# Kernel tuning notes

Hardware: AMD Instinct MI355X
Metric: run time of the kernel (lower is better)

Reference implementation:

```python
import jax, jax.numpy as jnp
import numpy as np

B, A, C, M = 4, 120000, 80, 32
ALPHA, GAMMA, EPS = 0.75, 2.0, 1e-4
STD = np.array([0.1, 0.1, 0.2, 0.2, 0.1, 0.1, 0.2, 0.2], dtype=np.float32)


def _make_boxes(key, shape, img=1024.0):
    k1, k2, k3, k4 = jax.random.split(key, 4)
    cx = jax.random.uniform(k1, shape) * img
    cy = jax.random.uniform(k2, shape) * img
    w = jax.random.uniform(k3, shape) * 224.0 + 32.0
    h = jax.random.uniform(k4, shape) * 224.0 + 32.0
    return jnp.stack([cx - 0.5 * w, cy - 0.5 * h, cx + 0.5 * w, cy + 0.5 * h], axis=-1)


def setup_inputs() -> dict:
    key = jax.random.key(0)
    kc, kr, ka, kh, kf, kl, ki = jax.random.split(key, 7)
    classifications = jax.random.uniform(kc, (B, A, C), dtype=jnp.float32)
    regressions = jax.random.normal(kr, (B, A, 8), dtype=jnp.float32)
    anchors = _make_boxes(ka, (1, A))  # [1,A,4]
    head = _make_boxes(kh, (B, M))     # [B,M,4]
    full = _make_boxes(kf, (B, M))     # [B,M,4]
    labels = jax.random.randint(kl, (B, M, 1), 0, C).astype(jnp.float32)
    ignore = jax.random.randint(ki, (B, M, 1), 0, 2).astype(jnp.float32)
    annotations = jnp.concatenate([head, full, labels, ignore], axis=-1)  # [B,M,10]
    return {"classifications": classifications, "regressions": regressions,
            "anchors": anchors, "annotations": annotations}


def _calc_iou(a, b):
    # a: [A,4], b: [B,M,4] -> [B,A,M]
    area_b = (b[..., 2] - b[..., 0]) * (b[..., 3] - b[..., 1])  # [B,M]
    a = a[None, :, None, :]
    bb = b[:, None, :, :]
    iw = jnp.clip(jnp.minimum(a[..., 2], bb[..., 2]) - jnp.maximum(a[..., 0], bb[..., 0]), 0.0)
    ih = jnp.clip(jnp.minimum(a[..., 3], bb[..., 3]) - jnp.maximum(a[..., 1], bb[..., 1]), 0.0)
    area_a = ((a[..., 2] - a[..., 0]) * (a[..., 3] - a[..., 1]))  # [1,A,1]
    inter = iw * ih
    ua = jnp.clip(area_a + area_b[:, None, :] - inter, 1e-8)
    return inter / ua


def reference(classifications, regressions, anchors, annotations):
    anchor = anchors[0]                       # [A,4]
    aw = anchor[:, 2] - anchor[:, 0]
    ah = anchor[:, 3] - anchor[:, 1]
    acx = anchor[:, 0] + 0.5 * aw
    acy = anchor[:, 1] + 0.5 * ah

    ann = annotations[..., :-1]               # [B,M,9]
    full_box = ann[..., 4:8]

    iou = _calc_iou(anchor, full_box)         # [B,A,M]
    iou_max = jnp.max(iou, axis=-1)           # [B,A]
    iou_arg = jnp.argmax(iou, axis=-1)        # [B,A]

    pos = iou_max >= 0.5                      # [B,A]
    neg = iou_max < 0.4
    num_pos = jnp.sum(pos, axis=1).astype(jnp.float32)  # [B]

    assigned = jnp.take_along_axis(ann, iou_arg[..., None], axis=1)  # [B,A,9]
    assigned_cls = assigned[..., 8].astype(jnp.int32)                # [B,A]

    one_hot = jax.nn.one_hot(assigned_cls, classifications.shape[-1], dtype=jnp.float32)
    targets = jnp.where(pos[..., None], one_hot,
                        jnp.where(neg[..., None], 0.0, -1.0))        # [B,A,C]

    p = jnp.clip(classifications, EPS, 1.0 - EPS)
    alpha_f = jnp.where(targets == 1.0, ALPHA, 1.0 - ALPHA)
    focal_w = alpha_f * jnp.where(targets == 1.0, 1.0 - p, p) ** GAMMA
    bce = -(targets * jnp.log(p) + (1.0 - targets) * jnp.log(1.0 - p))
    cls_loss = jnp.where(targets != -1.0, focal_w * bce, 0.0)
    cls_losses = jnp.sum(cls_loss, axis=(1, 2)) / jnp.clip(num_pos, 1.0)  # [B]

    gw_h = assigned[..., 2] - assigned[..., 0]
    gh_h = assigned[..., 3] - assigned[..., 1]
    gcx_h = assigned[..., 0] + 0.5 * gw_h
    gcy_h = assigned[..., 1] + 0.5 * gh_h
    gw_f = assigned[..., 6] - assigned[..., 4]
    gh_f = assigned[..., 7] - assigned[..., 5]
    gcx_f = assigned[..., 4] + 0.5 * gw_f
    gcy_f = assigned[..., 5] + 0.5 * gh_f
    gw_h = jnp.clip(gw_h, 1.0); gh_h = jnp.clip(gh_h, 1.0)
    gw_f = jnp.clip(gw_f, 1.0); gh_f = jnp.clip(gh_f, 1.0)

    t = jnp.stack([
        (gcx_f - acx) / aw, (gcy_f - acy) / ah,
        jnp.log(gw_f / aw), jnp.log(gh_f / ah),
        (gcx_h - acx) / aw * 4.0, (gcy_h - acy) / ah * 4.0,
        jnp.log(gw_h / aw * 4.0), jnp.log(gh_h / ah * 4.0),
    ], axis=-1) / jnp.asarray(STD)            # [B,A,8]

    diff = jnp.abs(t - regressions)
    # only_full=True: weights zero out cols 4:8
    diff = diff * jnp.asarray([1., 1., 1., 1., 0., 0., 0., 0.], dtype=jnp.float32)
    rl = jnp.where(diff <= 1.0 / 9.0, 0.5 * 9.0 * diff * diff, diff - 0.5 / 9.0)
    rl4 = rl[..., 0:4] * pos[..., None]       # [B,A,4], only positive anchors
    reg_losses = jnp.where(num_pos > 0,
                           jnp.sum(rl4, axis=(1, 2)) / (jnp.clip(num_pos, 1.0) * 4.0),
                           0.0)               # mean over positive rows x 4 cols

    return (jnp.mean(cls_losses, keepdims=True), jnp.mean(reg_losses, keepdims=True))
```

## Files before the change

kernel.cpp:

```cpp
#include <hip/hip_runtime.h>

#define NB 4
#define NA 120000
#define NC 80
#define NM 32

#define EPS_   1e-4f
#define LN2_   0.69314718055994531f

constexpr int BLOCK  = 256;
constexpr int WPB    = 4;
constexpr int APW    = 16;
constexpr int APC    = WPB * APW;
constexpr int NCHUNK = NA / APC;
constexpr int BPB    = 512;
constexpr int BINS   = 64;
constexpr int QCAP   = 256;

__device__ __forceinline__ float wave_reduce_f(float v) {
    #pragma unroll
    for (int off = 32; off > 0; off >>= 1) v += __shfl_down(v, off, 64);
    return v;
}
__device__ __forceinline__ double wave_reduce_d(double v) {
    #pragma unroll
    for (int off = 32; off > 0; off >>= 1) v += __shfl_down(v, off, 64);
    return v;
}

__device__ __forceinline__ float flog2(float x) { return __builtin_amdgcn_logf(x); }

__global__ __launch_bounds__(BLOCK, 4)
void focal_persist(const float* __restrict__ cls,
                   const float* __restrict__ reg,
                   const float* __restrict__ anchors,
                   const float* __restrict__ ann,
                   double* __restrict__ acc)
{
    __shared__ float s_ann[NM * 10];
    __shared__ float s_red[2][WPB];
    __shared__ int   s_q[QCAP];
    __shared__ int   s_qn;

    const int b    = blockIdx.x >> 9;
    const int blk  = blockIdx.x & (BPB - 1);
    const int tid  = threadIdx.x;
    const int wave = tid >> 6;
    const int lane = tid & 63;
    const int aloc = lane >> 2;
    const int part = lane & 3;

    if (tid == 0) s_qn = 0;
    s_ann[tid] = ann[b * NM * 10 + tid];
    if (tid < NM * 10 - BLOCK) s_ann[BLOCK + tid] = ann[b * NM * 10 + BLOCK + tid];
    __syncthreads();

    float clsSum = 0.0f, regLoss = 0.0f;

    const float4* anchors4 = (const float4*)anchors;
    const float4* cls4b    = (const float4*)cls + (size_t)b * NA * (NC / 4);

    int c = blk;
    float4 an0, x0, x1, x2, x3, x4_;
    {
        const int aw0 = c * APC + wave * APW;
        an0 = anchors4[aw0 + aloc];
        const float4* w4 = cls4b + (size_t)aw0 * (NC / 4);
        x0 = w4[lane]; x1 = w4[lane + 64]; x2 = w4[lane + 128];
        x3 = w4[lane + 192]; x4_ = w4[lane + 256];
    }

    while (c < NCHUNK) {
        const int cn = c + BPB;
        const int cl  = (cn < NCHUNK) ? cn : c;
        const int nw0 = cl * APC + wave * APW;
        const float4 an1 = anchors4[nw0 + aloc];
        const float4* v4 = cls4b + (size_t)nw0 * (NC / 4);
        const float4 y0 = v4[lane], y1 = v4[lane + 64], y2 = v4[lane + 128];
        const float4 y3 = v4[lane + 192], y4 = v4[lane + 256];

        const int a = c * APC + wave * APW + aloc;
        const float ax1 = an0.x, ay1 = an0.y, ax2 = an0.z, ay2 = an0.w;
        const float areaA = (ax2 - ax1) * (ay2 - ay1);

        float best = -1.0f;
        int   arg  = 0;
        #pragma unroll
        for (int i = 0; i < 8; ++i) {
            const int m = part * 8 + i;
            const float bx1 = s_ann[m * 10 + 4];
            const float by1 = s_ann[m * 10 + 5];
            const float bx2 = s_ann[m * 10 + 6];
            const float by2 = s_ann[m * 10 + 7];
            float iw = fminf(ax2, bx2) - fmaxf(ax1, bx1); iw = fmaxf(iw, 0.0f);
            float ih = fminf(ay2, by2) - fmaxf(ay1, by1); ih = fmaxf(ih, 0.0f);
            const float inter = iw * ih;
            const float areaB = (bx2 - bx1) * (by2 - by1);
            const float ua    = fmaxf(areaA + areaB - inter, 1e-8f);
            const float iou   = inter / ua;
            if (iou > best) { best = iou; arg = m; }
        }
        #pragma unroll
        for (int d = 1; d <= 2; d <<= 1) {
            const float ob = __shfl_xor(best, d, 64);
            const int   oa = __shfl_xor(arg,  d, 64);
            if (ob > best || (ob == best && oa < arg)) { best = ob; arg = oa; }
        }

        const bool pos = best >= 0.5f;
        const bool neg = best < 0.4f;
        const float coefL = (pos || neg) ? (-0.25f * LN2_) : 0.0f;

        if (pos && part == 0) {
            const int slot = atomicAdd(&s_qn, 1);
            s_q[slot] = (a << 5) | arg;
        }

        #define TERM(XV, J)                                                      \
        {                                                                        \
            const int idx = lane + 64 * (J);                                     \
            const float C = __shfl(coefL, (idx / (NC / 4)) << 2, 64);            \
            float p0 = fminf(fmaxf((XV).x, EPS_), 1.0f - EPS_);                  \
            float p1 = fminf(fmaxf((XV).y, EPS_), 1.0f - EPS_);                  \
            float p2 = fminf(fmaxf((XV).z, EPS_), 1.0f - EPS_);                  \
            float p3 = fminf(fmaxf((XV).w, EPS_), 1.0f - EPS_);                  \
            float t0 = p0 * p0 * flog2(1.0f - p0);                               \
            float t1 = p1 * p1 * flog2(1.0f - p1);                               \
            float t2 = p2 * p2 * flog2(1.0f - p2);                               \
            float t3 = p3 * p3 * flog2(1.0f - p3);                               \
            clsSum = fmaf((t0 + t1) + (t2 + t3), C, clsSum);                     \
        }
        TERM(x0, 0) TERM(x1, 1) TERM(x2, 2) TERM(x3, 3) TERM(x4_, 4)
        #undef TERM

        c = cn;
        an0 = an1; x0 = y0; x1 = y1; x2 = y2; x3 = y3; x4_ = y4;
    }

    __syncthreads();
    const int qn = s_qn;
    if (tid < qn) {
        const int e = s_q[tid];
        const int a = e >> 5;
        const int m = e & 31;

        const float4 an = anchors4[a];
        const float aw_ = an.z - an.x, ah = an.w - an.y;
        const float acx = an.x + 0.5f * aw_, acy = an.y + 0.5f * ah;

        const int cc = (int)s_ann[m * 10 + 8];
        const float xc = cls[((size_t)b * NA + a) * NC + cc];
        const float p  = fminf(fmaxf(xc, EPS_), 1.0f - EPS_);
        const float q  = 1.0f - p;
        clsSum += 0.75f * q * q * (-LN2_ * flog2(p))
                - 0.25f * p * p * (-LN2_ * flog2(q));

        const float fx1 = s_ann[m * 10 + 4];
        const float fy1 = s_ann[m * 10 + 5];
        const float fx2 = s_ann[m * 10 + 6];
        const float fy2 = s_ann[m * 10 + 7];
        float gw = fx2 - fx1, gh = fy2 - fy1;
        const float gcx = fx1 + 0.5f * gw, gcy = fy1 + 0.5f * gh;
        gw = fmaxf(gw, 1.0f); gh = fmaxf(gh, 1.0f);
        const float t0 = ((gcx - acx) / aw_) * 10.0f;
        const float t1 = ((gcy - acy) / ah)  * 10.0f;
        const float t2 = (LN2_ * flog2(gw / aw_)) * 5.0f;
        const float t3 = (LN2_ * flog2(gh / ah))  * 5.0f;
        const float4 r4 = ((const float4*)reg)[(size_t)(b * NA + a) * 2];
        const float d0 = fabsf(t0 - r4.x);
        const float d1 = fabsf(t1 - r4.y);
        const float d2 = fabsf(t2 - r4.z);
        const float d3 = fabsf(t3 - r4.w);
        const float beta = 1.0f / 9.0f;
        #define SL1(d) ((d) <= beta ? 4.5f * (d) * (d) : (d) - 0.5f / 9.0f)
        regLoss = SL1(d0) + SL1(d1) + SL1(d2) + SL1(d3);
        #undef SL1
    }

    float rc = wave_reduce_f(clsSum);
    float rr = wave_reduce_f(regLoss);
    if (lane == 0) { s_red[0][wave] = rc; s_red[1][wave] = rr; }
    __syncthreads();
    if (tid == 0) {
        const float cs = (s_red[0][0] + s_red[0][1]) + (s_red[0][2] + s_red[0][3]);
        const float rs = (s_red[1][0] + s_red[1][1]) + (s_red[1][2] + s_red[1][3]);
        const int bin = blockIdx.x & (BINS - 1);
        atomicAdd(&acc[(b * 3 + 0) * BINS + bin], (double)cs);
        atomicAdd(&acc[(b * 3 + 1) * BINS + bin], (double)rs);
        atomicAdd(&acc[(b * 3 + 2) * BINS + bin], (double)qn);
    }
}

__global__ void focal_finalize(const double* __restrict__ acc, float* __restrict__ out) {
    __shared__ double g[NB * 3];
    const int tid  = threadIdx.x;
    const int wave = tid >> 6, lane = tid & 63;
    double v = acc[wave * BINS + lane];
    v = wave_reduce_d(v);
    if (lane == 0) g[wave] = v;
    __syncthreads();
    if (tid == 0) {
        double clsTot = 0.0, regTot = 0.0;
        #pragma unroll
        for (int b = 0; b < NB; ++b) {
            const double np  = g[b * 3 + 2];
            const double npc = np < 1.0 ? 1.0 : np;
            clsTot += g[b * 3 + 0] / npc;
            regTot += (np > 0.0) ? g[b * 3 + 1] / (npc * 4.0) : 0.0;
        }
        out[0] = (float)(clsTot / NB);
        out[1] = (float)(regTot / NB);
    }
}

extern "C" void kernel_launch(void* const* d_in, const int* in_sizes, int n_in,
                              void* d_out, int out_size, void* d_ws, size_t ws_size,
                              hipStream_t stream) {
    const float* cls     = (const float*)d_in[0];
    const float* reg     = (const float*)d_in[1];
    const float* anchors = (const float*)d_in[2];
    const float* ann     = (const float*)d_in[3];
    float* out  = (float*)d_out;
    double* acc = (double*)d_ws;

    hipMemsetAsync(acc, 0, NB * 3 * BINS * sizeof(double), stream);

    focal_persist<<<NB * BPB, BLOCK, 0, stream>>>(cls, reg, anchors, ann, acc);
    focal_finalize<<<1, NB * 3 * BINS, 0, stream>>>(acc, out);
}
```

Baseline: 232.6 us.

## Use nontemporal class loads, drop software prefetch, replace atomics with per-block partials

The register double-buffered prefetch of the next chunk is removed. Class-probability loads now use nontemporal loads in a simple strided loop. The double atomic accumulation into bins and the memset are replaced by each block writing a float4 partial, which a finalize kernel reduces in double. This removes a memset launch and atomic traffic and lowers register pressure, but gives up the explicit load/compute overlap.

```diff
diff --git a/kernel.cpp b/kernel.cpp
--- a/kernel.cpp
+++ b/kernel.cpp
@@ -14,8 +14,13 @@
 constexpr int APC    = WPB * APW;
 constexpr int NCHUNK = NA / APC;
 constexpr int BPB    = 512;
-constexpr int BINS   = 64;
 constexpr int QCAP   = 256;
+
+typedef __attribute__((ext_vector_type(4))) float f32x4;
+
+__device__ __forceinline__ f32x4 nt_load4(const f32x4* p) {
+    return __builtin_nontemporal_load(p);
+}
 
 __device__ __forceinline__ float wave_reduce_f(float v) {
     #pragma unroll
@@ -35,7 +40,7 @@
                    const float* __restrict__ reg,
                    const float* __restrict__ anchors,
                    const float* __restrict__ ann,
-                   double* __restrict__ acc)
+                   float4* __restrict__ partials)
 {
     __shared__ float s_ann[NM * 10];
     __shared__ float s_red[2][WPB];
@@ -58,29 +63,21 @@
     float clsSum = 0.0f, regLoss = 0.0f;
 
     const float4* anchors4 = (const float4*)anchors;
-    const float4* cls4b    = (const float4*)cls + (size_t)b * NA * (NC / 4);
-
-    int c = blk;
-    float4 an0, x0, x1, x2, x3, x4_;
-    {
+    const f32x4*  cls4b    = (const f32x4*)cls + (size_t)b * NA * (NC / 4);
+
+    for (int c = blk; c < NCHUNK; c += BPB) {
         const int aw0 = c * APC + wave * APW;
-        an0 = anchors4[aw0 + aloc];
-        const float4* w4 = cls4b + (size_t)aw0 * (NC / 4);
-        x0 = w4[lane]; x1 = w4[lane + 64]; x2 = w4[lane + 128];
-        x3 = w4[lane + 192]; x4_ = w4[lane + 256];
-    }
-
-    while (c < NCHUNK) {
-        const int cn = c + BPB;
-        const int cl  = (cn < NCHUNK) ? cn : c;
-        const int nw0 = cl * APC + wave * APW;
-        const float4 an1 = anchors4[nw0 + aloc];
-        const float4* v4 = cls4b + (size_t)nw0 * (NC / 4);
-        const float4 y0 = v4[lane], y1 = v4[lane + 64], y2 = v4[lane + 128];
-        const float4 y3 = v4[lane + 192], y4 = v4[lane + 256];
-
-        const int a = c * APC + wave * APW + aloc;
-        const float ax1 = an0.x, ay1 = an0.y, ax2 = an0.z, ay2 = an0.w;
+        const int a   = aw0 + aloc;
+
+        const float4 an = anchors4[a];
+        const f32x4* w4 = cls4b + (size_t)aw0 * (NC / 4);
+        const f32x4 x0 = nt_load4(w4 + lane);
+        const f32x4 x1 = nt_load4(w4 + lane + 64);
+        const f32x4 x2 = nt_load4(w4 + lane + 128);
+        const f32x4 x3 = nt_load4(w4 + lane + 192);
+        const f32x4 x4_ = nt_load4(w4 + lane + 256);
+
+        const float ax1 = an.x, ay1 = an.y, ax2 = an.z, ay2 = an.w;
         const float areaA = (ax2 - ax1) * (ay2 - ay1);
 
         float best = -1.0f;
@@ -132,9 +129,6 @@
         }
         TERM(x0, 0) TERM(x1, 1) TERM(x2, 2) TERM(x3, 3) TERM(x4_, 4)
         #undef TERM
-
-        c = cn;
-        an0 = an1; x0 = y0; x1 = y1; x2 = y2; x3 = y3; x4_ = y4;
     }
 
     __syncthreads();
@@ -184,29 +178,34 @@
     if (tid == 0) {
         const float cs = (s_red[0][0] + s_red[0][1]) + (s_red[0][2] + s_red[0][3]);
         const float rs = (s_red[1][0] + s_red[1][1]) + (s_red[1][2] + s_red[1][3]);
-        const int bin = blockIdx.x & (BINS - 1);
-        atomicAdd(&acc[(b * 3 + 0) * BINS + bin], (double)cs);
-        atomicAdd(&acc[(b * 3 + 1) * BINS + bin], (double)rs);
-        atomicAdd(&acc[(b * 3 + 2) * BINS + bin], (double)qn);
-    }
-}
-
-__global__ void focal_finalize(const double* __restrict__ acc, float* __restrict__ out) {
-    __shared__ double g[NB * 3];
+        partials[blockIdx.x] = make_float4(cs, rs, (float)qn, 0.0f);
+    }
+}
+
+__global__ __launch_bounds__(BPB)
+void focal_finalize(const float4* __restrict__ partials, float* __restrict__ out) {
+    __shared__ double s[3][NB][BPB / 64];
     const int tid  = threadIdx.x;
     const int wave = tid >> 6, lane = tid & 63;
-    double v = acc[wave * BINS + lane];
-    v = wave_reduce_d(v);
-    if (lane == 0) g[wave] = v;
+    #pragma unroll
+    for (int b = 0; b < NB; ++b) {
+        const float4 p = partials[b * BPB + tid];
+        const double rc = wave_reduce_d((double)p.x);
+        const double rr = wave_reduce_d((double)p.y);
+        const double rn = wave_reduce_d((double)p.z);
+        if (lane == 0) { s[0][b][wave] = rc; s[1][b][wave] = rr; s[2][b][wave] = rn; }
+    }
     __syncthreads();
     if (tid == 0) {
         double clsTot = 0.0, regTot = 0.0;
         #pragma unroll
         for (int b = 0; b < NB; ++b) {
-            const double np  = g[b * 3 + 2];
-            const double npc = np < 1.0 ? 1.0 : np;
-            clsTot += g[b * 3 + 0] / npc;
-            regTot += (np > 0.0) ? g[b * 3 + 1] / (npc * 4.0) : 0.0;
+            double C = 0.0, R = 0.0, N = 0.0;
+            #pragma unroll
+            for (int w = 0; w < BPB / 64; ++w) { C += s[0][b][w]; R += s[1][b][w]; N += s[2][b][w]; }
+            const double npc = N < 1.0 ? 1.0 : N;
+            clsTot += C / npc;
+            regTot += (N > 0.0) ? R / (npc * 4.0) : 0.0;
         }
         out[0] = (float)(clsTot / NB);
         out[1] = (float)(regTot / NB);
@@ -220,11 +219,9 @@
     const float* reg     = (const float*)d_in[1];
     const float* anchors = (const float*)d_in[2];
     const float* ann     = (const float*)d_in[3];
-    float* out  = (float*)d_out;
-    double* acc = (double*)d_ws;
-
-    hipMemsetAsync(acc, 0, NB * 3 * BINS * sizeof(double), stream);
-
-    focal_persist<<<NB * BPB, BLOCK, 0, stream>>>(cls, reg, anchors, ann, acc);
-    focal_finalize<<<1, NB * 3 * BINS, 0, stream>>>(acc, out);
-}
+    float* out = (float*)d_out;
+    float4* partials = (float4*)d_ws;
+
+    focal_persist<<<NB * BPB, BLOCK, 0, stream>>>(cls, reg, anchors, ann, partials);
+    focal_finalize<<<1, BPB, 0, stream>>>(partials, out);
+}
```

Result: faster. 224.2 us (-3.6%).
